# Kernel optimization log

Measured on AMD Instinct MI355X. Metric: run time of the kernel, lower is better.

Reference implementation:

```python
import jax, jax.numpy as jnp
import numpy as np

SIGMA = 4.0
KSIZE = 2 * int(4.0 * SIGMA + 0.5) + 1  # 33, as in anomalib's GaussianBlur2d
INPUT_SIZE = (224, 224)
NUM_NEIGHBORS = 9


def avg_pool_4_1_1(x):
    # nn.AvgPool2d(kernel_size=4, stride=1, padding=1), count_include_pad=True -> divide by 16
    s = jax.lax.reduce_window(x, 0.0, jax.lax.add, (1, 1, 4, 4), (1, 1, 1, 1),
                              ((0, 0), (0, 0), (1, 1), (1, 1)))
    return s / 16.0


def gaussian_kernel1d(ksize, sigma):
    x = jnp.arange(ksize, dtype=jnp.float32) - (ksize - 1) / 2.0
    g = jnp.exp(-0.5 * (x / sigma) ** 2)
    return g / jnp.sum(g)


def gaussian_blur(x):
    # separable 33x33 gaussian blur, reflect padding (kornia GaussianBlur2d default)
    k = gaussian_kernel1d(KSIZE, SIGMA)
    pad = KSIZE // 2
    xp = jnp.pad(x, ((0, 0), (0, 0), (pad, pad), (pad, pad)), mode='reflect')
    dn = ('NCHW', 'OIHW', 'NCHW')
    y = jax.lax.conv_general_dilated(xp, k.reshape(1, 1, KSIZE, 1), (1, 1), 'VALID', dimension_numbers=dn)
    y = jax.lax.conv_general_dilated(y, k.reshape(1, 1, 1, KSIZE), (1, 1), 'VALID', dimension_numbers=dn)
    return y


def euclidean_dist(x, y):
    # pairwise L2: x [..., n, d], y [..., m, d] -> [..., n, m]
    x2 = jnp.sum(x * x, axis=-1, keepdims=True)
    y2 = jnp.sum(y * y, axis=-1, keepdims=True)
    d2 = x2 - 2.0 * jnp.matmul(x, jnp.swapaxes(y, -1, -2)) + jnp.swapaxes(y2, -1, -2)
    return jnp.sqrt(jnp.clip(d2, 0.0, None))


def compute_anomaly_score(patch_scores, locations, embedding, memory_bank):
    # PatchCore re-weighting (num_neighbors > 1 branch)
    B, P = patch_scores.shape
    bidx = jnp.arange(B)
    max_patches = jnp.argmax(patch_scores, axis=1)                      # [B]
    feats = embedding.reshape(B, P, -1)[bidx, max_patches]              # [B, C]
    score = patch_scores[bidx, max_patches]                             # [B] s*
    nn_index = locations[bidx, max_patches]                             # [B]
    nn_sample = memory_bank[nn_index]                                   # [B, C]
    d_bank = euclidean_dist(nn_sample, memory_bank)                     # [B, M]
    _, support = jax.lax.top_k(-d_bank, NUM_NEIGHBORS)                  # [B, K] smallest
    support_feats = memory_bank[support]                                # [B, K, C]
    distances = euclidean_dist(feats[:, None, :], support_feats)        # [B, 1, K]
    weights = 1.0 - jnp.exp(score) / jnp.sum(jnp.exp(distances[:, 0, :]), axis=-1)
    return weights * score


def setup_inputs() -> dict:
    key = jax.random.key(0)
    k1, k2, k3 = jax.random.split(key, 3)
    feat_layer2 = jax.random.normal(k1, (8, 512, 28, 28), dtype=jnp.float32)
    feat_layer3 = jax.random.normal(k2, (8, 1024, 14, 14), dtype=jnp.float32)
    memory_bank = jax.random.normal(k3, (32000, 1536), dtype=jnp.float32)
    return {"feat_layer2": feat_layer2, "feat_layer3": feat_layer3, "memory_bank": memory_bank}


def reference(feat_layer2, feat_layer3, memory_bank):
    # feature_pooler = AvgPool2d(4,1,1)
    f2 = avg_pool_4_1_1(feat_layer2)   # [B, 512, 27, 27]
    f3 = avg_pool_4_1_1(feat_layer3)   # [B, 1024, 13, 13]
    B, _, H, W = f2.shape
    # generate_embedding: bilinear upsample layer3 to layer2 size, concat channels
    f3u = jax.image.resize(f3, (B, f3.shape[1], H, W), method='bilinear')
    emb = jnp.concatenate([f2, f3u], axis=1)                            # [B, 1536, 27, 27]
    C = emb.shape[1]
    embedding = jnp.transpose(emb, (0, 2, 3, 1)).reshape(-1, C)         # [B*H*W, C]
    # nearest_neighbors with n_neighbors=1 over the coreset memory bank
    d = euclidean_dist(embedding, memory_bank)                          # [B*H*W, M]
    patch_scores = jnp.min(d, axis=1).reshape(B, -1)
    locations = jnp.argmin(d, axis=1).reshape(B, -1)
    pred_score = compute_anomaly_score(patch_scores, locations, embedding, memory_bank)
    # anomaly map: upsample patch scores to input size + gaussian blur
    pmap = patch_scores.reshape(B, 1, H, W)
    amap = jax.image.resize(pmap, (B, 1, INPUT_SIZE[0], INPUT_SIZE[1]), method='bilinear')
    anomaly_map = gaussian_blur(amap)
    return anomaly_map, pred_score
```

## Files before the change

### kernel.cpp

```cpp
#include <hip/hip_runtime.h>
#include <math.h>

#define NB 8
#define C2 512
#define C3 1024
#define HIN2 28
#define HIN3 14
#define HO2 27
#define HO3 13
#define CC 1536
#define NP (NB*HO2*HO2)
#define NM 32000
#define NKNN 9
#define OH 224
#define AMAP_N (NB*OH*OH)

#define BM 256
#define BN 256
#define BK 64
#define KT (CC/BK)
#define MB_CNT ((NP+BM-1)/BM)
#define NB_CNT (NM/BN)
#define NWG (MB_CNT*NB_CNT)

typedef unsigned long long u64;
typedef unsigned int u32;
typedef __attribute__((ext_vector_type(8))) short bf16x8;
typedef __attribute__((ext_vector_type(4))) float f32x4;

struct GW { float w[33]; };

__device__ __forceinline__ float warp_sum(float v){
  #pragma unroll
  for (int off=32; off; off>>=1) v += __shfl_down(v, off);
  return v;
}

__device__ __forceinline__ ushort f2bf(float f){
  u32 u = __float_as_uint(f);
  u32 r = (u + 0x7FFFu + ((u>>16)&1u)) >> 16;
  return (ushort)r;
}
__device__ __forceinline__ float bf2f(ushort b){
  return __uint_as_float(((u32)b)<<16);
}

#define GLDS(g, l) __builtin_amdgcn_global_load_lds((const __attribute__((address_space(1))) void*)(g), (__attribute__((address_space(3))) void*)(l), 16, 0, 0)
#define WAITVM0() asm volatile("s_waitcnt vmcnt(0)" ::: "memory")
#define SB0() __builtin_amdgcn_sched_barrier(0)
__device__ __forceinline__ void bar_raw(){
  asm volatile("" ::: "memory");
  __builtin_amdgcn_s_barrier();
  asm volatile("" ::: "memory");
}

__global__ __launch_bounds__(256) void k_avgpool2(const float* __restrict__ in, ushort* __restrict__ embB){
  __shared__ float pl[16*789];
  int b = blockIdx.x >> 5, cg = blockIdx.x & 31;
  const float4* src = (const float4*)(in + ((size_t)b*C2 + cg*16)*(HIN2*HIN2));
  for (int idx = threadIdx.x; idx < 16*196; idx += 256){
    int c = idx/196, p4 = idx - c*196;
    float4 v = src[idx];
    float* d = &pl[c*789 + p4*4];
    d[0]=v.x; d[1]=v.y; d[2]=v.z; d[3]=v.w;
  }
  __syncthreads();
  int c = threadIdx.x & 15, g = threadIdx.x >> 4;
  for (int pos = g; pos < HO2*HO2; pos += 16){
    int i = pos/HO2, j = pos - i*HO2;
    const float* p = &pl[c*789];
    float s = 0.f;
    #pragma unroll
    for (int di=0; di<4; ++di){
      int y = i - 1 + di;
      if ((unsigned)y >= HIN2) continue;
      #pragma unroll
      for (int dj=0; dj<4; ++dj){
        int x = j - 1 + dj;
        if ((unsigned)x < HIN2) s += p[y*HIN2 + x];
      }
    }
    embB[((size_t)((b*HO2 + i)*HO2 + j))*CC + cg*16 + c] = f2bf(s * (1.f/16.f));
  }
}

__global__ __launch_bounds__(256) void k_avgpool3(const float* __restrict__ in, float* __restrict__ f3p){
  __shared__ float pl[64*197];
  int b = blockIdx.x >> 4, cg = blockIdx.x & 15;
  const float4* src = (const float4*)(in + ((size_t)b*C3 + cg*64)*(HIN3*HIN3));
  for (int idx = threadIdx.x; idx < 64*49; idx += 256){
    int c = idx/49, p4 = idx - c*49;
    float4 v = src[idx];
    float* d = &pl[c*197 + p4*4];
    d[0]=v.x; d[1]=v.y; d[2]=v.z; d[3]=v.w;
  }
  __syncthreads();
  int c = threadIdx.x & 63, g = threadIdx.x >> 6;
  for (int pos = g; pos < HO3*HO3; pos += 4){
    int i = pos/HO3, j = pos - i*HO3;
    const float* p = &pl[c*197];
    float s = 0.f;
    #pragma unroll
    for (int di=0; di<4; ++di){
      int y = i - 1 + di;
      if ((unsigned)y >= HIN3) continue;
      #pragma unroll
      for (int dj=0; dj<4; ++dj){
        int x = j - 1 + dj;
        if ((unsigned)x < HIN3) s += p[y*HIN3 + x];
      }
    }
    f3p[((size_t)((b*HO3 + i)*HO3 + j))*C3 + cg*64 + c] = s * (1.f/16.f);
  }
}

__global__ void k_upsample3(const float* __restrict__ f3p, ushort* __restrict__ embB){
  int t = blockIdx.x*256 + threadIdx.x;
  if (t >= NB*HO2*HO2*C3) return;
  int c = t % C3; int r = t / C3;
  int ox = r % HO2; r /= HO2;
  int oy = r % HO2; int b = r / HO2;
  float fy = (oy + 0.5f) * (13.f/27.f) - 0.5f;
  float fx = (ox + 0.5f) * (13.f/27.f) - 0.5f;
  int y0 = (int)floorf(fy); float wy = fy - (float)y0;
  int x0 = (int)floorf(fx); float wx = fx - (float)x0;
  int y0c = min(max(y0,0), HO3-1), y1c = min(max(y0+1,0), HO3-1);
  int x0c = min(max(x0,0), HO3-1), x1c = min(max(x0+1,0), HO3-1);
  const float* base = f3p + (size_t)(b*HO3*HO3)*C3;
  float v00 = base[(size_t)(y0c*HO3 + x0c)*C3 + c];
  float v01 = base[(size_t)(y0c*HO3 + x1c)*C3 + c];
  float v10 = base[(size_t)(y1c*HO3 + x0c)*C3 + c];
  float v11 = base[(size_t)(y1c*HO3 + x1c)*C3 + c];
  float v = (1.f-wy)*((1.f-wx)*v00 + wx*v01) + wy*((1.f-wx)*v10 + wx*v11);
  embB[((size_t)((b*HO2 + oy)*HO2 + ox))*CC + C2 + c] = f2bf(v);
}

__global__ void k_bank_prep(const float* __restrict__ bank, ushort* __restrict__ bankB,
                            float* __restrict__ y2){
  int wave = threadIdx.x >> 6, lane = threadIdx.x & 63;
  int r = blockIdx.x*4 + wave;
  if (r >= NM) return;
  const float4* p = (const float4*)(bank + (size_t)r*CC);
  ushort4* q = (ushort4*)(bankB + (size_t)r*CC);
  float s = 0.f;
  #pragma unroll
  for (int it=0; it<6; ++it){
    float4 v = p[it*64 + lane];
    s += v.x*v.x + v.y*v.y + v.z*v.z + v.w*v.w;
    ushort4 o; o.x = f2bf(v.x); o.y = f2bf(v.y); o.z = f2bf(v.z); o.w = f2bf(v.w);
    q[it*64 + lane] = o;
  }
  s = warp_sum(s);
  if (lane==0) y2[r] = s;
}

__global__ void k_rowsumsq_bf(const ushort* __restrict__ src, float* __restrict__ dst, int rows,
                              u64* __restrict__ packed){
  int wave = threadIdx.x >> 6;
  int lane = threadIdx.x & 63;
  int r = blockIdx.x*4 + wave;
  if (r >= rows) return;
  const uint4* p = (const uint4*)(src + (size_t)r*CC);
  float s = 0.f;
  #pragma unroll
  for (int it=0; it<3; ++it){
    uint4 v = p[it*64 + lane];
    u32 ws_[4] = {v.x, v.y, v.z, v.w};
    #pragma unroll
    for (int q=0;q<4;q++){
      float lo = __uint_as_float(ws_[q]<<16);
      float hi = __uint_as_float(ws_[q]&0xFFFF0000u);
      s += lo*lo + hi*hi;
    }
  }
  s = warp_sum(s);
  if (lane==0){ dst[r] = s; packed[r] = ~0ull; }
}

__global__ __launch_bounds__(512, 2) void k_distmin_mfma(
    const ushort* __restrict__ A, const ushort* __restrict__ B,
    const float* __restrict__ x2, const float* __restrict__ y2,
    u64* __restrict__ packed)
{
  __shared__ ushort smem[4*BM*BK];
  ushort* As0 = smem;
  ushort* Bs0 = smem + BM*BK;
  ushort* As1 = smem + 2*BM*BK;
  ushort* Bs1 = smem + 3*BM*BK;

  const int tid = threadIdx.x;
  const int w   = tid >> 6;
  const int l   = tid & 63;
  const int wr  = w >> 2;
  const int wc  = w & 3;
  const int ccol = l & 15;
  const int cgrp = l >> 4;

  int orig = blockIdx.x;
  const int q8 = NWG/8, r8 = NWG%8;
  int xcd = orig & 7, sidx = orig >> 3;
  int wg = (xcd < r8 ? xcd*(q8+1) : r8*(q8+1) + (xcd-r8)*q8) + sidx;
  const int mb = wg % MB_CNT;
  const int nb = wg / MB_CNT;
  const int m0 = mb * BM;
  const int n0 = nb * BN;

  const int rowin = l >> 3;
  const int scol  = (((l&7) ^ rowin) * 8);
  int chA1[2], chA2[2], chB1[2], chB2[2];
  u32 aO1[2], aO2[2], bO1[2], bO2[2];
  u32 lA1[2], lA2[2], lB1[2], lB2[2];
  #pragma unroll
  for (int c=0;c<2;c++){
    chA1[c] = (w<4) ? (2*w+c) : (8+2*w+c);
    chA2[c] = chA1[c] + 8;
    chB1[c] = (w>>1)*8 + (w&1)*2 + c;
    chB2[c] = chB1[c] + 4;
    aO1[c] = (u32)min(m0 + chA1[c]*8 + rowin, NP-1)*CC + scol;
    aO2[c] = (u32)min(m0 + chA2[c]*8 + rowin, NP-1)*CC + scol;
    bO1[c] = (u32)(n0 + chB1[c]*8 + rowin)*CC + scol;
    bO2[c] = (u32)(n0 + chB2[c]*8 + rowin)*CC + scol;
    lA1[c] = (u32)chA1[c]*1024 + l*16;
    lA2[c] = (u32)chA2[c]*1024 + l*16;
    lB1[c] = (u32)chB1[c]*1024 + l*16;
    lB2[c] = (u32)chB2[c]*1024 + l*16;
  }

  const u32 o0 = (u32)((cgrp ^ (ccol & 7)) * 8);
  u32 aRow[8], bRow[4];
  #pragma unroll
  for (int mi=0;mi<8;mi++) aRow[mi] = (u32)(wr*128 + mi*16 + ccol)*BK;
  #pragma unroll
  for (int ni=0;ni<4;ni++) bRow[ni] = (u32)(wc*64 + ni*16 + ccol)*BK;

  f32x4 acc[8][4];
  #pragma unroll
  for (int mi=0;mi<8;mi++)
    #pragma unroll
    for (int ni=0;ni<4;ni++)
      acc[mi][ni] = (f32x4){0.f,0.f,0.f,0.f};

  bf16x8 rA[8][2], rB[4][2];

  #pragma unroll
  for (int c=0;c<2;c++){
    GLDS(A + aO1[c], (char*)As0 + lA1[c]);
    GLDS(A + aO2[c], (char*)As0 + lA2[c]);
    GLDS(B + bO1[c], (char*)Bs0 + lB1[c]);
    GLDS(B + bO2[c], (char*)Bs0 + lB2[c]);
  }
  WAITVM0(); bar_raw(); SB0();
  #pragma unroll
  for (int mi=0;mi<8;mi++)
    #pragma unroll
    for (int ks=0;ks<2;ks++)
      rA[mi][ks] = *(const bf16x8*)&As0[aRow[mi] + (o0 ^ (u32)(ks<<5))];
  #pragma unroll
  for (int ni=0;ni<4;ni++)
    #pragma unroll
    for (int ks=0;ks<2;ks++)
      rB[ni][ks] = *(const bf16x8*)&Bs0[bRow[ni] + (o0 ^ (u32)(ks<<5))];

  #pragma unroll 1
  for (int kt=0; kt<KT; ++kt){
    const u32 kk = (u32)(kt+1)*BK;
    ushort* nA = (kt & 1) ? As0 : As1;
    ushort* nB = (kt & 1) ? Bs0 : Bs1;

    if (kt+1 < KT){
      #pragma unroll
      for (int c=0;c<2;c++){
        GLDS(A + aO1[c] + kk, (char*)nA + lA1[c]);
        GLDS(A + aO2[c] + kk, (char*)nA + lA2[c]);
        GLDS(B + bO1[c] + kk, (char*)nB + lB1[c]);
        GLDS(B + bO2[c] + kk, (char*)nB + lB2[c]);
      }
    }
    SB0();

    __builtin_amdgcn_s_setprio(1);
    #pragma unroll
    for (int mi=0;mi<8;mi++)
      #pragma unroll
      for (int ni=0;ni<4;ni++)
        #pragma unroll
        for (int ks=0;ks<2;ks++)
          acc[mi][ni] = __builtin_amdgcn_mfma_f32_16x16x32_bf16(rA[mi][ks], rB[ni][ks], acc[mi][ni], 0, 0, 0);
    __builtin_amdgcn_s_setprio(0);

    WAITVM0();
    bar_raw();
    SB0();

    #pragma unroll
    for (int mi=0;mi<8;mi++)
      #pragma unroll
      for (int ks=0;ks<2;ks++)
        rA[mi][ks] = *(const bf16x8*)&nA[aRow[mi] + (o0 ^ (u32)(ks<<5))];
    #pragma unroll
    for (int ni=0;ni<4;ni++)
      #pragma unroll
      for (int ks=0;ks<2;ks++)
        rB[ni][ks] = *(const bf16x8*)&nB[bRow[ni] + (o0 ^ (u32)(ks<<5))];
  }

  float xv[8][4];
  #pragma unroll
  for (int mi=0;mi<8;mi++)
    #pragma unroll
    for (int r=0;r<4;r++)
      xv[mi][r] = x2[min(m0 + wr*128 + mi*16 + cgrp*4 + r, NP-1)];

  u64 best[8][4];
  #pragma unroll
  for (int mi=0;mi<8;mi++)
    #pragma unroll
    for (int r=0;r<4;r++) best[mi][r] = ~0ull;

  #pragma unroll
  for (int ni=0;ni<4;ni++){
    const int n = n0 + wc*64 + ni*16 + ccol;
    const float yy = y2[n];
    #pragma unroll
    for (int mi=0;mi<8;mi++)
      #pragma unroll
      for (int r=0;r<4;r++){
        float d2 = fmaxf(xv[mi][r] + yy - 2.f*acc[mi][ni][r], 0.f);
        u64 pk = (((u64)__float_as_uint(d2))<<32) | (u32)n;
        if (pk < best[mi][r]) best[mi][r] = pk;
      }
  }

  #pragma unroll
  for (int mi=0;mi<8;mi++)
    #pragma unroll
    for (int r=0;r<4;r++){
      u64 pk = best[mi][r];
      #pragma unroll
      for (int md=1; md<16; md<<=1){
        u64 o = __shfl_xor(pk, md);
        if (o < pk) pk = o;
      }
      const int row = m0 + wr*128 + mi*16 + cgrp*4 + r;
      if (ccol==0 && row < NP) atomicMin(&packed[row], pk);
    }
}

__global__ void k_finalize(const u64* __restrict__ packed, float* __restrict__ patch_d,
                           int* __restrict__ sel_mp, float* __restrict__ sel_score, int* __restrict__ sel_nn){
  int b = blockIdx.x;
  int tid = threadIdx.x;
  __shared__ u64 red[4];
  u64 best = 0;
  for (int p = tid; p < HO2*HO2; p += 256){
    u64 v = packed[b*HO2*HO2 + p];
    float d = sqrtf(__uint_as_float((u32)(v>>32)));
    patch_d[b*HO2*HO2 + p] = d;
    u64 pk = (((u64)__float_as_uint(d))<<32) | (u32)(HO2*HO2 - p);
    if (pk > best) best = pk;
  }
  int lane = tid & 63, w = tid >> 6;
  #pragma unroll
  for (int d=32; d; d>>=1){ u64 o = __shfl_down(best, d); if (o > best) best = o; }
  if (lane==0) red[w] = best;
  __syncthreads();
  if (tid==0){
    u64 bb = red[0];
    for (int q=1;q<4;q++) if (red[q] > bb) bb = red[q];
    int p = HO2*HO2 - (int)(bb & 0xffffffffu);
    sel_mp[b] = p;
    sel_score[b] = __uint_as_float((u32)(bb>>32));
    sel_nn[b] = (int)(packed[b*HO2*HO2 + p] & 0xffffffffu);
  }
}

__device__ __forceinline__ void bf8dec(uint4 v, float* f){
  u32 a[4] = {v.x, v.y, v.z, v.w};
  #pragma unroll
  for (int q=0;q<4;q++){
    f[2*q]   = __uint_as_float(a[q]<<16);
    f[2*q+1] = __uint_as_float(a[q]&0xFFFF0000u);
  }
}

__global__ __launch_bounds__(256) void k_dbank(const ushort* __restrict__ bankB, const float* __restrict__ y2,
    const int* __restrict__ sel_nn, float* __restrict__ d_bank){
  int wave = threadIdx.x >> 6, lane = threadIdx.x & 63;
  int m = blockIdx.x*4 + wave;
  if (m >= NM) return;
  int nn[NB];
  #pragma unroll
  for (int b=0;b<NB;b++) nn[b] = sel_nn[b];
  const uint4* pm = (const uint4*)(bankB + (size_t)m*CC);
  float acc[NB];
  #pragma unroll
  for (int b=0;b<NB;b++) acc[b] = 0.f;
  #pragma unroll
  for (int it=0; it<3; ++it){
    uint4 v = pm[it*64 + lane];
    float vf[8]; bf8dec(v, vf);
    #pragma unroll
    for (int b=0;b<NB;b++){
      uint4 u = ((const uint4*)(bankB + (size_t)nn[b]*CC))[it*64 + lane];
      float uf[8]; bf8dec(u, uf);
      #pragma unroll
      for (int q=0;q<8;q++) acc[b] += vf[q]*uf[q];
    }
  }
  #pragma unroll
  for (int b=0;b<NB;b++){
    float s = warp_sum(acc[b]);
    if (lane==0) d_bank[(size_t)b*NM + m] = fmaxf(y2[nn[b]] + y2[m] - 2.f*s, 0.f);
  }
}

__global__ __launch_bounds__(256) void k_top9_part(const float* __restrict__ d_bank, u64* __restrict__ part9){
  int b = blockIdx.x >> 5, seg = blockIdx.x & 31;
  int tid = threadIdx.x;
  __shared__ u64 cand[256*NKNN];
  __shared__ u64 red[4];
  __shared__ u64 gbest_s;
  u64 t9[NKNN];
  #pragma unroll
  for (int q=0;q<NKNN;q++) t9[q] = ~0ull;
  int base = seg*1000;
  for (int i = tid; i < 1000; i += 256){
    int m = base + i;
    float v = d_bank[(size_t)b*NM + m];
    u64 pk = (((u64)__float_as_uint(v))<<32) | (u32)m;
    if (pk < t9[NKNN-1]){
      t9[NKNN-1] = pk;
      #pragma unroll
      for (int q=NKNN-1; q>0; --q){
        if (t9[q] < t9[q-1]){ u64 tt=t9[q]; t9[q]=t9[q-1]; t9[q-1]=tt; }
      }
    }
  }
  #pragma unroll
  for (int q=0;q<NKNN;q++) cand[tid*NKNN+q] = t9[q];
  __syncthreads();
  int lane = tid & 63, w = tid >> 6;
  for (int k=0;k<NKNN;++k){
    u64 mybest = ~0ull;
    #pragma unroll
    for (int q=0;q<NKNN;q++){ u64 v = cand[tid*NKNN+q]; if (v < mybest) mybest = v; }
    u64 rb = mybest;
    #pragma unroll
    for (int d=32; d; d>>=1){ u64 o = __shfl_down(rb, d); if (o < rb) rb = o; }
    if (lane==0) red[w] = rb;
    __syncthreads();
    if (tid==0){
      u64 bb = red[0];
      for (int q=1;q<4;q++) if (red[q] < bb) bb = red[q];
      gbest_s = bb;
      part9[((size_t)b*32 + seg)*NKNN + k] = bb;
    }
    __syncthreads();
    u64 gb = gbest_s;
    #pragma unroll
    for (int q=0;q<NKNN;q++) if (cand[tid*NKNN+q] == gb) cand[tid*NKNN+q] = ~0ull;
    __syncthreads();
  }
}

__global__ __launch_bounds__(256) void k_score_final(const u64* __restrict__ part9, const float* __restrict__ bank,
    const ushort* __restrict__ embB, const float* __restrict__ x2, const float* __restrict__ y2,
    const int* __restrict__ sel_mp, const float* __restrict__ sel_score, float* __restrict__ out_score){
  int b = blockIdx.x, tid = threadIdx.x;
  __shared__ u64 cand[32*NKNN];
  __shared__ int sel[NKNN];
  __shared__ u64 red[4];
  __shared__ u64 gbest_s;
  __shared__ float fred[4];
  __shared__ float sumexp_s;
  for (int i = tid; i < 32*NKNN; i += 256) cand[i] = part9[(size_t)b*32*NKNN + i];
  __syncthreads();
  int lane = tid & 63, w = tid >> 6;
  for (int k=0;k<NKNN;++k){
    u64 mybest = ~0ull;
    for (int i = tid; i < 32*NKNN; i += 256){ u64 v = cand[i]; if (v < mybest) mybest = v; }
    u64 rb = mybest;
    #pragma unroll
    for (int d=32; d; d>>=1){ u64 o = __shfl_down(rb, d); if (o < rb) rb = o; }
    if (lane==0) red[w] = rb;
    __syncthreads();
    if (tid==0){
      u64 bb = red[0];
      for (int q=1;q<4;q++) if (red[q] < bb) bb = red[q];
      gbest_s = bb;
      sel[k] = (int)(bb & 0xffffffffu);
    }
    __syncthreads();
    u64 gb = gbest_s;
    for (int i = tid; i < 32*NKNN; i += 256) if (cand[i] == gb) cand[i] = ~0ull;
    __syncthreads();
  }

  int mp = sel_mp[b];
  const ushort* fv = embB + (size_t)(b*HO2*HO2 + mp)*CC;
  float fx2 = x2[b*HO2*HO2 + mp];
  if (tid==0) sumexp_s = 0.f;
  __syncthreads();
  for (int k=0;k<NKNN;++k){
    const float* sv = bank + (size_t)sel[k]*CC;
    float part = 0.f;
    for (int i = tid; i < CC; i += 256) part += bf2f(fv[i])*sv[i];
    part = warp_sum(part);
    if (lane==0) fred[w] = part;
    __syncthreads();
    if (tid==0){
      float dot = fred[0]+fred[1]+fred[2]+fred[3];
      float d2 = fmaxf(fx2 + y2[sel[k]] - 2.f*dot, 0.f);
      sumexp_s += expf(sqrtf(d2));
    }
    __syncthreads();
  }
  if (tid==0){
    float s = sel_score[b];
    out_score[b] = (1.f - expf(s)/sumexp_s) * s;
  }
}

__global__ __launch_bounds__(256) void k_amap_fused(const float* __restrict__ patch_d,
    float* __restrict__ out, GW gw){
  __shared__ float Ts[OH*HO2];
  __shared__ float ps[HO2*HO2];
  __shared__ float tmp[HO2*OH];
  int b = blockIdx.x, t = threadIdx.x;
  for (int idx=t; idx<OH*HO2; idx+=256){
    int x = idx / HO2, j = idx - x*HO2;
    float s = 0.f;
    #pragma unroll
    for (int k=0;k<33;++k){
      int yy = x + k - 16;
      yy = (yy < 0) ? -yy : yy;
      yy = (yy > OH-1) ? (2*(OH-1) - yy) : yy;
      float fy = (yy + 0.5f) * (27.f/224.f) - 0.5f;
      int y0 = (int)floorf(fy); float wy = fy - (float)y0;
      int j0 = min(max(y0,0), HO2-1), j1 = min(max(y0+1,0), HO2-1);
      float c = ((j==j0)?(1.f-wy):0.f) + ((j==j1)?wy:0.f);
      s += gw.w[k]*c;
    }
    Ts[idx] = s;
  }
  for (int idx=t; idx<HO2*HO2; idx+=256) ps[idx] = patch_d[b*HO2*HO2+idx];
  __syncthreads();
  for (int idx=t; idx<HO2*OH; idx+=256){
    int i = idx/OH, x = idx - i*OH;
    float s = 0.f;
    #pragma unroll
    for (int j=0;j<HO2;j++) s += ps[i*HO2+j]*Ts[x*HO2+j];
    tmp[i*OH+x] = s;
  }
  __syncthreads();
  for (int idx=t; idx<OH*OH; idx+=256){
    int y = idx/OH, x = idx - y*OH;
    float s = 0.f;
    #pragma unroll
    for (int i=0;i<HO2;i++) s += Ts[y*HO2+i]*tmp[i*OH+x];
    out[(size_t)b*OH*OH + idx] = s;
  }
}

extern "C" void kernel_launch(void* const* d_in, const int* in_sizes, int n_in,
                              void* d_out, int out_size, void* d_ws, size_t ws_size,
                              hipStream_t stream){
  const float* f2   = (const float*)d_in[0];
  const float* f3   = (const float*)d_in[1];
  const float* bank = (const float*)d_in[2];
  float* out = (float*)d_out;

  char* ws = (char*)d_ws;
  size_t off = 0;
  auto alloc = [&](size_t bytes)->char*{ char* p = ws + off; off += (bytes + 255) & ~(size_t)255; return p; };
  ushort* embB    = (ushort*)alloc((size_t)NP*CC*2);
  ushort* bankB   = (ushort*)alloc((size_t)NM*CC*2);
  float* f3p      = (float*)alloc((size_t)NB*HO3*HO3*C3*4);
  float* y2       = (float*)alloc((size_t)NM*4);
  float* x2       = (float*)alloc((size_t)NP*4);
  u64*   packed   = (u64*)  alloc((size_t)NP*8);
  float* patch_d  = (float*)alloc((size_t)NP*4);
  float* d_bank   = (float*)alloc((size_t)NB*NM*4);
  u64*   part9    = (u64*)  alloc((size_t)NB*32*NKNN*8);
  int*   sel_mp   = (int*)  alloc(NB*4);
  float* sel_scr  = (float*)alloc(NB*4);
  int*   sel_nn   = (int*)  alloc(NB*4);

  GW gw;
  { float s=0.f; for(int i=0;i<33;i++){ float xx=(float)i-16.f; gw.w[i]=expf(-0.5f*(xx/4.f)*(xx/4.f)); s+=gw.w[i]; }
    for(int i=0;i<33;i++) gw.w[i]/=s; }

  k_avgpool2<<<NB*32,256,0,stream>>>(f2, embB);
  k_avgpool3<<<NB*16,256,0,stream>>>(f3, f3p);
  k_upsample3<<<(NB*HO2*HO2*C3+255)/256,256,0,stream>>>(f3p, embB);
  k_bank_prep<<<(NM+3)/4,256,0,stream>>>(bank, bankB, y2);
  k_rowsumsq_bf<<<(NP+3)/4,256,0,stream>>>(embB, x2, NP, packed);
  k_distmin_mfma<<<NWG,512,0,stream>>>(embB, bankB, x2, y2, packed);
  k_finalize<<<NB,256,0,stream>>>(packed, patch_d, sel_mp, sel_scr, sel_nn);
  k_dbank<<<(NM+3)/4,256,0,stream>>>(bankB, y2, sel_nn, d_bank);
  k_top9_part<<<NB*32,256,0,stream>>>(d_bank, part9);
  k_score_final<<<NB,256,0,stream>>>(part9, bank, embB, x2, y2, sel_mp, sel_scr, out + AMAP_N);
  k_amap_fused<<<NB,256,0,stream>>>(patch_d, out, gw);
}
```

Measured before the change: 944.9 us.

## Use 4 waves per block with 128x128 per-wave tiles in distmin GEMM

The fused distance-min GEMM kernel moves from 8 waves (each computing a 128x64 sub-tile) to 4 waves (each computing 128x128), keeping the 256x256 block tile. Each wave now issues twice as many MFMAs per fragment load, raising arithmetic intensity per LDS read, and the epilogue reduces across ni in registers before the shuffle reduction. The cost is a doubled accumulator register footprint (256 VGPRs for acc), one block per CU, and fewer waves to hide load latency. Each thread also now issues all 8 global-to-LDS copies per stage.

```diff
diff --git a/kernel.cpp b/kernel.cpp
--- a/kernel.cpp
+++ b/kernel.cpp
@@ -177,7 +177,7 @@
   if (lane==0){ dst[r] = s; packed[r] = ~0ull; }
 }
 
-__global__ __launch_bounds__(512, 2) void k_distmin_mfma(
+__global__ __launch_bounds__(256, 1) void k_distmin_mfma(
     const ushort* __restrict__ A, const ushort* __restrict__ B,
     const float* __restrict__ x2, const float* __restrict__ y2,
     u64* __restrict__ packed)
@@ -191,8 +191,8 @@
   const int tid = threadIdx.x;
   const int w   = tid >> 6;
   const int l   = tid & 63;
-  const int wr  = w >> 2;
-  const int wc  = w & 3;
+  const int wr  = w >> 1;
+  const int wc  = w & 1;
   const int ccol = l & 15;
   const int cgrp = l >> 4;
 
@@ -207,47 +207,36 @@
 
   const int rowin = l >> 3;
   const int scol  = (((l&7) ^ rowin) * 8);
-  int chA1[2], chA2[2], chB1[2], chB2[2];
-  u32 aO1[2], aO2[2], bO1[2], bO2[2];
-  u32 lA1[2], lA2[2], lB1[2], lB2[2];
-  #pragma unroll
-  for (int c=0;c<2;c++){
-    chA1[c] = (w<4) ? (2*w+c) : (8+2*w+c);
-    chA2[c] = chA1[c] + 8;
-    chB1[c] = (w>>1)*8 + (w&1)*2 + c;
-    chB2[c] = chB1[c] + 4;
-    aO1[c] = (u32)min(m0 + chA1[c]*8 + rowin, NP-1)*CC + scol;
-    aO2[c] = (u32)min(m0 + chA2[c]*8 + rowin, NP-1)*CC + scol;
-    bO1[c] = (u32)(n0 + chB1[c]*8 + rowin)*CC + scol;
-    bO2[c] = (u32)(n0 + chB2[c]*8 + rowin)*CC + scol;
-    lA1[c] = (u32)chA1[c]*1024 + l*16;
-    lA2[c] = (u32)chA2[c]*1024 + l*16;
-    lB1[c] = (u32)chB1[c]*1024 + l*16;
-    lB2[c] = (u32)chB2[c]*1024 + l*16;
+  u32 aOf[8], bOf[8], lAo[8], lBo[8];
+  #pragma unroll
+  for (int c=0;c<8;c++){
+    int ch = w*8 + c;
+    aOf[c] = (u32)min(m0 + ch*8 + rowin, NP-1)*CC + scol;
+    bOf[c] = (u32)(n0 + ch*8 + rowin)*CC + scol;
+    lAo[c] = (u32)ch*1024 + l*16;
+    lBo[c] = (u32)ch*1024 + l*16;
   }
 
   const u32 o0 = (u32)((cgrp ^ (ccol & 7)) * 8);
-  u32 aRow[8], bRow[4];
+  u32 aRow[8], bRow[8];
   #pragma unroll
   for (int mi=0;mi<8;mi++) aRow[mi] = (u32)(wr*128 + mi*16 + ccol)*BK;
   #pragma unroll
-  for (int ni=0;ni<4;ni++) bRow[ni] = (u32)(wc*64 + ni*16 + ccol)*BK;
-
-  f32x4 acc[8][4];
+  for (int ni=0;ni<8;ni++) bRow[ni] = (u32)(wc*128 + ni*16 + ccol)*BK;
+
+  f32x4 acc[8][8];
   #pragma unroll
   for (int mi=0;mi<8;mi++)
     #pragma unroll
-    for (int ni=0;ni<4;ni++)
+    for (int ni=0;ni<8;ni++)
       acc[mi][ni] = (f32x4){0.f,0.f,0.f,0.f};
 
-  bf16x8 rA[8][2], rB[4][2];
-
-  #pragma unroll
-  for (int c=0;c<2;c++){
-    GLDS(A + aO1[c], (char*)As0 + lA1[c]);
-    GLDS(A + aO2[c], (char*)As0 + lA2[c]);
-    GLDS(B + bO1[c], (char*)Bs0 + lB1[c]);
-    GLDS(B + bO2[c], (char*)Bs0 + lB2[c]);
+  bf16x8 rA[8][2], rB[8][2];
+
+  #pragma unroll
+  for (int c=0;c<8;c++){
+    GLDS(A + aOf[c], (char*)As0 + lAo[c]);
+    GLDS(B + bOf[c], (char*)Bs0 + lBo[c]);
   }
   WAITVM0(); bar_raw(); SB0();
   #pragma unroll
@@ -256,7 +245,7 @@
     for (int ks=0;ks<2;ks++)
       rA[mi][ks] = *(const bf16x8*)&As0[aRow[mi] + (o0 ^ (u32)(ks<<5))];
   #pragma unroll
-  for (int ni=0;ni<4;ni++)
+  for (int ni=0;ni<8;ni++)
     #pragma unroll
     for (int ks=0;ks<2;ks++)
       rB[ni][ks] = *(const bf16x8*)&Bs0[bRow[ni] + (o0 ^ (u32)(ks<<5))];
@@ -269,11 +258,9 @@
 
     if (kt+1 < KT){
       #pragma unroll
-      for (int c=0;c<2;c++){
-        GLDS(A + aO1[c] + kk, (char*)nA + lA1[c]);
-        GLDS(A + aO2[c] + kk, (char*)nA + lA2[c]);
-        GLDS(B + bO1[c] + kk, (char*)nB + lB1[c]);
-        GLDS(B + bO2[c] + kk, (char*)nB + lB2[c]);
+      for (int c=0;c<8;c++){
+        GLDS(A + aOf[c] + kk, (char*)nA + lAo[c]);
+        GLDS(B + bOf[c] + kk, (char*)nB + lBo[c]);
       }
     }
     SB0();
@@ -282,7 +269,7 @@
     #pragma unroll
     for (int mi=0;mi<8;mi++)
       #pragma unroll
-      for (int ni=0;ni<4;ni++)
+      for (int ni=0;ni<8;ni++)
         #pragma unroll
         for (int ks=0;ks<2;ks++)
           acc[mi][ni] = __builtin_amdgcn_mfma_f32_16x16x32_bf16(rA[mi][ks], rB[ni][ks], acc[mi][ni], 0, 0, 0);
@@ -298,52 +285,37 @@
       for (int ks=0;ks<2;ks++)
         rA[mi][ks] = *(const bf16x8*)&nA[aRow[mi] + (o0 ^ (u32)(ks<<5))];
     #pragma unroll
-    for (int ni=0;ni<4;ni++)
+    for (int ni=0;ni<8;ni++)
       #pragma unroll
       for (int ks=0;ks<2;ks++)
         rB[ni][ks] = *(const bf16x8*)&nB[bRow[ni] + (o0 ^ (u32)(ks<<5))];
   }
 
-  float xv[8][4];
-  #pragma unroll
-  for (int mi=0;mi<8;mi++)
-    #pragma unroll
-    for (int r=0;r<4;r++)
-      xv[mi][r] = x2[min(m0 + wr*128 + mi*16 + cgrp*4 + r, NP-1)];
-
-  u64 best[8][4];
-  #pragma unroll
-  for (int mi=0;mi<8;mi++)
-    #pragma unroll
-    for (int r=0;r<4;r++) best[mi][r] = ~0ull;
-
-  #pragma unroll
-  for (int ni=0;ni<4;ni++){
-    const int n = n0 + wc*64 + ni*16 + ccol;
-    const float yy = y2[n];
-    #pragma unroll
-    for (int mi=0;mi<8;mi++)
-      #pragma unroll
-      for (int r=0;r<4;r++){
-        float d2 = fmaxf(xv[mi][r] + yy - 2.f*acc[mi][ni][r], 0.f);
-        u64 pk = (((u64)__float_as_uint(d2))<<32) | (u32)n;
-        if (pk < best[mi][r]) best[mi][r] = pk;
+  float yy[8];
+  #pragma unroll
+  for (int ni=0;ni<8;ni++) yy[ni] = y2[n0 + wc*128 + ni*16 + ccol];
+
+  #pragma unroll
+  for (int mi=0;mi<8;mi++){
+    #pragma unroll
+    for (int r=0;r<4;r++){
+      const int row = m0 + wr*128 + mi*16 + cgrp*4 + r;
+      const float xv = x2[min(row, NP-1)];
+      u64 pk = ~0ull;
+      #pragma unroll
+      for (int ni=0;ni<8;ni++){
+        float d2 = fmaxf(xv + yy[ni] - 2.f*acc[mi][ni][r], 0.f);
+        u64 c = (((u64)__float_as_uint(d2))<<32) | (u32)(n0 + wc*128 + ni*16 + ccol);
+        if (c < pk) pk = c;
       }
-  }
-
-  #pragma unroll
-  for (int mi=0;mi<8;mi++)
-    #pragma unroll
-    for (int r=0;r<4;r++){
-      u64 pk = best[mi][r];
       #pragma unroll
       for (int md=1; md<16; md<<=1){
         u64 o = __shfl_xor(pk, md);
         if (o < pk) pk = o;
       }
-      const int row = m0 + wr*128 + mi*16 + cgrp*4 + r;
       if (ccol==0 && row < NP) atomicMin(&packed[row], pk);
     }
+  }
 }
 
 __global__ void k_finalize(const u64* __restrict__ packed, float* __restrict__ patch_d,
@@ -595,7 +567,7 @@
   k_upsample3<<<(NB*HO2*HO2*C3+255)/256,256,0,stream>>>(f3p, embB);
   k_bank_prep<<<(NM+3)/4,256,0,stream>>>(bank, bankB, y2);
   k_rowsumsq_bf<<<(NP+3)/4,256,0,stream>>>(embB, x2, NP, packed);
-  k_distmin_mfma<<<NWG,512,0,stream>>>(embB, bankB, x2, y2, packed);
+  k_distmin_mfma<<<NWG,256,0,stream>>>(embB, bankB, x2, y2, packed);
   k_finalize<<<NB,256,0,stream>>>(packed, patch_d, sel_mp, sel_scr, sel_nn);
   k_dbank<<<(NM+3)/4,256,0,stream>>>(bankB, y2, sel_nn, d_bank);
   k_top9_part<<<NB*32,256,0,stream>>>(d_bank, part9);
```

After: 2.360 ms. 150% more time.

## Split GEMM mainloop into quadrant phases with staggered global-to-LDS prefetch

Applied to the files above, without the earlier changes.

Restructures the bf16 MFMA distance GEMM main loop into eight phases per two K-tiles. Each phase loads a quarter of the A/B fragments from LDS, issues one chunk of the next tile's global_load_lds, and runs a quadrant of MFMAs. Partial vmcnt waits keep loads in flight across iterations, so memory traffic is spread out and overlaps the MFMA work instead of being issued as one burst. In exchange it adds many more barriers per tile and relies on delicate LDS hazard ordering (clamped redundant loads at the tail).

```diff
diff --git a/kernel.cpp b/kernel.cpp
--- a/kernel.cpp
+++ b/kernel.cpp
@@ -47,6 +47,8 @@
 
 #define GLDS(g, l) __builtin_amdgcn_global_load_lds((const __attribute__((address_space(1))) void*)(g), (__attribute__((address_space(3))) void*)(l), 16, 0, 0)
 #define WAITVM0() asm volatile("s_waitcnt vmcnt(0)" ::: "memory")
+#define WAITVM6() asm volatile("s_waitcnt vmcnt(6)" ::: "memory")
+#define WAITLGKM0() asm volatile("s_waitcnt lgkmcnt(0)" ::: "memory")
 #define SB0() __builtin_amdgcn_sched_barrier(0)
 __device__ __forceinline__ void bar_raw(){
   asm volatile("" ::: "memory");
@@ -187,6 +189,8 @@
   ushort* Bs0 = smem + BM*BK;
   ushort* As1 = smem + 2*BM*BK;
   ushort* Bs1 = smem + 3*BM*BK;
+  char* As0c = (char*)As0; char* Bs0c = (char*)Bs0;
+  char* As1c = (char*)As1; char* Bs1c = (char*)Bs1;
 
   const int tid = threadIdx.x;
   const int w   = tid >> 6;
@@ -240,69 +244,84 @@
     for (int ni=0;ni<4;ni++)
       acc[mi][ni] = (f32x4){0.f,0.f,0.f,0.f};
 
-  bf16x8 rA[8][2], rB[4][2];
-
-  #pragma unroll
-  for (int c=0;c<2;c++){
-    GLDS(A + aO1[c], (char*)As0 + lA1[c]);
-    GLDS(A + aO2[c], (char*)As0 + lA2[c]);
-    GLDS(B + bO1[c], (char*)Bs0 + lB1[c]);
-    GLDS(B + bO2[c], (char*)Bs0 + lB2[c]);
-  }
-  WAITVM0(); bar_raw(); SB0();
-  #pragma unroll
-  for (int mi=0;mi<8;mi++)
-    #pragma unroll
-    for (int ks=0;ks<2;ks++)
-      rA[mi][ks] = *(const bf16x8*)&As0[aRow[mi] + (o0 ^ (u32)(ks<<5))];
-  #pragma unroll
-  for (int ni=0;ni<4;ni++)
-    #pragma unroll
-    for (int ks=0;ks<2;ks++)
-      rB[ni][ks] = *(const bf16x8*)&Bs0[bRow[ni] + (o0 ^ (u32)(ks<<5))];
+  bf16x8 rAlo[4][2], rAhi[4][2], rBlo[2][2], rBhi[2][2];
+
+#define STG(P, GO, BASE, LO, KK) { GLDS((P)+GO[0]+(KK), (BASE)+LO[0]); GLDS((P)+GO[1]+(KK), (BASE)+LO[1]); }
+#define RD_ALO(S) { _Pragma("unroll") for (int mi=0;mi<4;mi++) _Pragma("unroll") for (int ks=0;ks<2;ks++) rAlo[mi][ks] = *(const bf16x8*)&(S)[aRow[mi] + (o0 ^ (u32)(ks<<5))]; }
+#define RD_AHI(S) { _Pragma("unroll") for (int mi=0;mi<4;mi++) _Pragma("unroll") for (int ks=0;ks<2;ks++) rAhi[mi][ks] = *(const bf16x8*)&(S)[aRow[mi+4] + (o0 ^ (u32)(ks<<5))]; }
+#define RD_BLO(S) { _Pragma("unroll") for (int ni=0;ni<2;ni++) _Pragma("unroll") for (int ks=0;ks<2;ks++) rBlo[ni][ks] = *(const bf16x8*)&(S)[bRow[ni] + (o0 ^ (u32)(ks<<5))]; }
+#define RD_BHI(S) { _Pragma("unroll") for (int ni=0;ni<2;ni++) _Pragma("unroll") for (int ks=0;ks<2;ks++) rBhi[ni][ks] = *(const bf16x8*)&(S)[bRow[ni+2] + (o0 ^ (u32)(ks<<5))]; }
+#define MM_Q00 { _Pragma("unroll") for (int mi=0;mi<4;mi++) _Pragma("unroll") for (int ni=0;ni<2;ni++) _Pragma("unroll") for (int ks=0;ks<2;ks++) acc[mi][ni]     = __builtin_amdgcn_mfma_f32_16x16x32_bf16(rAlo[mi][ks], rBlo[ni][ks], acc[mi][ni],     0,0,0); }
+#define MM_Q01 { _Pragma("unroll") for (int mi=0;mi<4;mi++) _Pragma("unroll") for (int ni=0;ni<2;ni++) _Pragma("unroll") for (int ks=0;ks<2;ks++) acc[mi][ni+2]   = __builtin_amdgcn_mfma_f32_16x16x32_bf16(rAlo[mi][ks], rBhi[ni][ks], acc[mi][ni+2],   0,0,0); }
+#define MM_Q10 { _Pragma("unroll") for (int mi=0;mi<4;mi++) _Pragma("unroll") for (int ni=0;ni<2;ni++) _Pragma("unroll") for (int ks=0;ks<2;ks++) acc[mi+4][ni]   = __builtin_amdgcn_mfma_f32_16x16x32_bf16(rAhi[mi][ks], rBlo[ni][ks], acc[mi+4][ni],   0,0,0); }
+#define MM_Q11 { _Pragma("unroll") for (int mi=0;mi<4;mi++) _Pragma("unroll") for (int ni=0;ni<2;ni++) _Pragma("unroll") for (int ks=0;ks<2;ks++) acc[mi+4][ni+2] = __builtin_amdgcn_mfma_f32_16x16x32_bf16(rAhi[mi][ks], rBhi[ni][ks], acc[mi+4][ni+2], 0,0,0); }
+#define PRIO1 __builtin_amdgcn_s_setprio(1)
+#define PRIO0 __builtin_amdgcn_s_setprio(0)
+
+  STG(A, aO1, As0c, lA1, 0u);
+  STG(B, bO1, Bs0c, lB1, 0u);
+  STG(B, bO2, Bs0c, lB2, 0u);
+  STG(A, aO2, As0c, lA2, 0u);
+  STG(A, aO1, As1c, lA1, (u32)BK);
+  STG(B, bO1, Bs1c, lB1, (u32)BK);
+  STG(B, bO2, Bs1c, lB2, (u32)BK);
+  WAITVM6(); bar_raw(); SB0();
 
   #pragma unroll 1
-  for (int kt=0; kt<KT; ++kt){
-    const u32 kk = (u32)(kt+1)*BK;
-    ushort* nA = (kt & 1) ? As0 : As1;
-    ushort* nB = (kt & 1) ? Bs0 : Bs1;
-
-    if (kt+1 < KT){
-      #pragma unroll
-      for (int c=0;c<2;c++){
-        GLDS(A + aO1[c] + kk, (char*)nA + lA1[c]);
-        GLDS(A + aO2[c] + kk, (char*)nA + lA2[c]);
-        GLDS(B + bO1[c] + kk, (char*)nB + lB1[c]);
-        GLDS(B + bO2[c] + kk, (char*)nB + lB2[c]);
-      }
-    }
-    SB0();
-
-    __builtin_amdgcn_s_setprio(1);
-    #pragma unroll
-    for (int mi=0;mi<8;mi++)
-      #pragma unroll
-      for (int ni=0;ni<4;ni++)
-        #pragma unroll
-        for (int ks=0;ks<2;ks++)
-          acc[mi][ni] = __builtin_amdgcn_mfma_f32_16x16x32_bf16(rA[mi][ks], rB[ni][ks], acc[mi][ni], 0, 0, 0);
-    __builtin_amdgcn_s_setprio(0);
-
-    WAITVM0();
-    bar_raw();
-    SB0();
-
-    #pragma unroll
-    for (int mi=0;mi<8;mi++)
-      #pragma unroll
-      for (int ks=0;ks<2;ks++)
-        rA[mi][ks] = *(const bf16x8*)&nA[aRow[mi] + (o0 ^ (u32)(ks<<5))];
-    #pragma unroll
-    for (int ni=0;ni<4;ni++)
-      #pragma unroll
-      for (int ks=0;ks<2;ks++)
-        rB[ni][ks] = *(const bf16x8*)&nB[bRow[ni] + (o0 ^ (u32)(ks<<5))];
-  }
+  for (int it=0; it<KT/2; ++it){
+    const u32 kk1 = (u32)(2*it+1)*BK;
+    const u32 kk2 = (u32)min(2*it+2, KT-1)*BK;
+    const u32 kk3 = (u32)min(2*it+3, KT-1)*BK;
+
+    RD_ALO(As0); RD_BLO(Bs0);
+    STG(A, aO2, As1c, lA2, kk1);
+    bar_raw(); WAITLGKM0(); SB0();
+    PRIO1; MM_Q00; PRIO0;
+    bar_raw();
+
+    RD_BHI(Bs0);
+    STG(A, aO1, As0c, lA1, kk2);
+    bar_raw(); WAITLGKM0(); SB0();
+    PRIO1; MM_Q01; PRIO0;
+    bar_raw();
+
+    RD_AHI(As0);
+    STG(B, bO1, Bs0c, lB1, kk2);
+    bar_raw(); WAITLGKM0(); SB0();
+    PRIO1; MM_Q10; PRIO0;
+    bar_raw();
+
+    STG(B, bO2, Bs0c, lB2, kk2);
+    bar_raw(); SB0();
+    PRIO1; MM_Q11; PRIO0;
+    WAITVM6();
+    bar_raw();
+
+    RD_ALO(As1); RD_BLO(Bs1);
+    STG(A, aO2, As0c, lA2, kk2);
+    bar_raw(); WAITLGKM0(); SB0();
+    PRIO1; MM_Q00; PRIO0;
+    bar_raw();
+
+    RD_BHI(Bs1);
+    STG(A, aO1, As1c, lA1, kk3);
+    bar_raw(); WAITLGKM0(); SB0();
+    PRIO1; MM_Q01; PRIO0;
+    bar_raw();
+
+    RD_AHI(As1);
+    STG(B, bO1, Bs1c, lB1, kk3);
+    bar_raw(); WAITLGKM0(); SB0();
+    PRIO1; MM_Q10; PRIO0;
+    bar_raw();
+
+    STG(B, bO2, Bs1c, lB2, kk3);
+    bar_raw(); SB0();
+    PRIO1; MM_Q11; PRIO0;
+    WAITVM6();
+    bar_raw();
+  }
+  WAITVM0();
 
   float xv[8][4];
   #pragma unroll
```

Result: no change. 963.2 us (+1.9%).
